# Performance work log

Measured on AMD Instinct MI355X. Metric: run time of the kernel, lower is better.

## Reference

```python
import jax, jax.numpy as jnp
import numpy as np

B, S, D, H = 2, 2048, 1024, 16
DH = D // H          # 64, even -> RoPE valid
ROPE_BASE = 10000.0
LN_EPS = 1e-5


def _rope_cache(seq_len, head_dim, dtype):
    half = head_dim // 2
    inv_freq = 1.0 / (ROPE_BASE ** (jnp.arange(half, dtype=jnp.float32) / half))
    t = jnp.arange(seq_len, dtype=jnp.float32)
    freqs = t[:, None] * inv_freq[None, :]            # [S, half]
    emb = jnp.concatenate([freqs, freqs], axis=-1)    # [S, DH]
    return jnp.cos(emb).astype(dtype)[None, None], jnp.sin(emb).astype(dtype)[None, None]


def _rotate_every_two(x):
    x_even = x[..., ::2]
    x_odd = x[..., 1::2]
    return jnp.stack([-x_odd, x_even], axis=-1).reshape(x.shape)


def setup_inputs() -> dict:
    key = jax.random.key(0)
    ks = jax.random.split(key, 4)
    w = lambda k, shape: (jax.random.normal(k, shape, jnp.float32) * 0.02)
    return {
        "x_qk": jax.random.normal(ks[0], (B, S, D), jnp.float32),
        "x_v": jax.random.normal(ks[1], (B, S, D), jnp.float32),
        "W_qk": w(ks[2], (D, 2 * D)),
        "b_qk": jnp.zeros((2 * D,), jnp.float32),
        "W_v": w(ks[3], (D, D)),
        "b_v": jnp.zeros((D,), jnp.float32),
        "ln_gamma": jnp.ones((D,), jnp.float32),
        "ln_beta": jnp.zeros((D,), jnp.float32),
    }


def reference(x_qk, x_v, W_qk, b_qk, W_v, b_v, ln_gamma, ln_beta):
    b, s, d = x_qk.shape
    # fused QK projection -> [B,S,2,H,DH]
    qk = (x_qk @ W_qk + b_qk).reshape(b, s, 2, H, DH)
    q = jnp.transpose(qk[:, :, 0], (0, 2, 1, 3))  # [B,H,S,DH]
    k = jnp.transpose(qk[:, :, 1], (0, 2, 1, 3))
    v = jnp.transpose((x_v @ W_v + b_v).reshape(b, s, H, DH), (0, 2, 1, 3))

    cos, sin = _rope_cache(s, DH, q.dtype)
    q = q * cos + _rotate_every_two(q) * sin
    k = k * cos + _rotate_every_two(k) * sin

    scale = 1.0 / jnp.sqrt(jnp.asarray(DH, q.dtype))
    scores = jnp.einsum("bhqd,bhkd->bhqk", q, k) * scale
    probs = jax.nn.softmax(scores, axis=-1)
    attn = jnp.einsum("bhqk,bhkd->bhqd", probs, v)      # [B,H,S,DH]
    attn = jnp.transpose(attn, (0, 2, 1, 3)).reshape(b, s, d)

    mu = jnp.mean(attn, axis=-1, keepdims=True)
    var = jnp.var(attn, axis=-1, keepdims=True)
    out = (attn - mu) * jax.lax.rsqrt(var + LN_EPS) * ln_gamma + ln_beta
    return out
```

## Files before the change

kernel.cpp:

```cpp
#include <hip/hip_runtime.h>
#include <hip/hip_bf16.h>

#define Bn 2
#define Sn 2048
#define Dn 1024
#define Hn 16
#define DHn 64
#define Kd 1024
#define Mn (Bn * Sn)
#define LN10K 9.210340371976184f

typedef __attribute__((ext_vector_type(8))) short bf16x8;
typedef __attribute__((ext_vector_type(4))) float f32x4;
typedef __attribute__((ext_vector_type(16))) float f32x16;

static __device__ __forceinline__ ushort f2bf(float f) {
    uint u = __float_as_uint(f);
    u += 0x7fff + ((u >> 16) & 1);
    return (ushort)(u >> 16);
}
static __device__ __forceinline__ uint cvtpk(float a, float b) {
    uint r;
    asm("v_cvt_pk_bf16_f32 %0, %1, %2" : "=v"(r) : "v"(a), "v"(b));
    return r;
}
static __device__ __forceinline__ void plswap(uint& a, uint& b) {
    asm volatile("v_permlane32_swap_b32 %0, %1" : "+v"(a), "+v"(b));
}

#define MFMA16(a, b, c) __builtin_amdgcn_mfma_f32_16x16x32_bf16((a), (b), (c), 0, 0, 0)
#define MFMA32(a, b, c) __builtin_amdgcn_mfma_f32_32x32x16_bf16((a), (b), (c), 0, 0, 0)

static __device__ __forceinline__ void gload16(const ushort* g, ushort* l) {
    __builtin_amdgcn_global_load_lds(
        (const __attribute__((address_space(1))) void*)g,
        (__attribute__((address_space(3))) void*)l, 16, 0, 0);
}

static __device__ __forceinline__ int swz(int row, int col16) {
    return row * 128 + (((col16) * 16) ^ ((row & 7) << 4));
}

__global__ __launch_bounds__(256) void rope_tab(float* __restrict__ ct,
                                                float* __restrict__ st)
{
    const int idx = blockIdx.x * 256 + threadIdx.x;
    const int s = idx >> 5, fe = idx & 31;
    const float f = expf(-LN10K * (float)fe / 32.0f);
    const float a = (float)s * f;
    ct[idx] = cosf(a);
    st[idx] = sinf(a);
}

__global__ __launch_bounds__(256) void cvt_bf16(const float* __restrict__ in,
                                                ushort* __restrict__ out)
{
    const size_t i = ((size_t)blockIdx.x * 256 + threadIdx.x) * 8;
    const float4 a = *(const float4*)(in + i);
    const float4 b = *(const float4*)(in + i + 4);
    ushort4 lo = make_ushort4(f2bf(a.x), f2bf(a.y), f2bf(a.z), f2bf(a.w));
    ushort4 hi = make_ushort4(f2bf(b.x), f2bf(b.y), f2bf(b.z), f2bf(b.w));
    *(ushort4*)(out + i) = lo;
    *(ushort4*)(out + i + 4) = hi;
}

__global__ __launch_bounds__(256) void transpose_bf16(
    const float* __restrict__ in, ushort* __restrict__ out, int R, int C)
{
    __shared__ ushort t[32][33];
    const int n0 = blockIdx.x * 32, k0 = blockIdx.y * 32;
    const int x = threadIdx.x, y = threadIdx.y;
#pragma unroll
    for (int i = 0; i < 4; ++i)
        t[y + 8 * i][x] = f2bf(in[(size_t)(k0 + y + 8 * i) * C + n0 + x]);
    __syncthreads();
#pragma unroll
    for (int i = 0; i < 4; ++i)
        out[(size_t)(n0 + y + 8 * i) * R + k0 + x] = t[x][y + 8 * i];
}

template <int MODE>
__global__ __launch_bounds__(256) void gemm_mfma(
    const ushort* __restrict__ A, const ushort* __restrict__ Bt,
    const float* __restrict__ bias, const float* __restrict__ ctab,
    const float* __restrict__ stab, ushort* __restrict__ o0,
    ushort* __restrict__ o1)
{
    __shared__ ushort Asm[128 * 64];
    __shared__ ushort Bsm[128 * 64];

    const int tid = threadIdx.x;
    const int lane = tid & 63, w = tid >> 6;
    const int g = lane >> 4, c = lane & 15;
    const int mbase = blockIdx.y * 128;
    const int nbase = blockIdx.x * 128;
    const int wm = (w >> 1) * 64, wn = (w & 1) * 64;

    f32x4 acc[4][4];
#pragma unroll
    for (int mf = 0; mf < 4; ++mf)
#pragma unroll
        for (int nf = 0; nf < 4; ++nf)
            acc[mf][nf] = (f32x4){0.f, 0.f, 0.f, 0.f};

    const int sbase = w * 64 + lane;

    for (int k0 = 0; k0 < Kd; k0 += 64) {
#pragma unroll
        for (int j = 0; j < 4; ++j) {
            const int i = j * 256 + sbase;
            const int row = i >> 3, c16 = i & 7;
            const int kc = (c16 ^ (row & 7)) * 8;
            gload16(A + (size_t)(mbase + row) * Kd + k0 + kc,
                    &Asm[(size_t)(j * 256 + w * 64) * 8]);
            gload16(Bt + (size_t)(nbase + row) * Kd + k0 + kc,
                    &Bsm[(size_t)(j * 256 + w * 64) * 8]);
        }
        __syncthreads();

#pragma unroll
        for (int ks = 0; ks < 2; ++ks) {
            bf16x8 af[4], bfr[4];
#pragma unroll
            for (int mf = 0; mf < 4; ++mf) {
                const int row = wm + mf * 16 + c;
                af[mf] = *(const bf16x8*)((const char*)Asm + swz(row, ks * 4 + g));
            }
#pragma unroll
            for (int nf = 0; nf < 4; ++nf) {
                const int row = wn + nf * 16 + c;
                bfr[nf] = *(const bf16x8*)((const char*)Bsm + swz(row, ks * 4 + g));
            }
#pragma unroll
            for (int mf = 0; mf < 4; ++mf)
#pragma unroll
                for (int nf = 0; nf < 4; ++nf)
                    acc[mf][nf] = MFMA16(af[mf], bfr[nf], acc[mf][nf]);
        }
        __syncthreads();
    }

#pragma unroll
    for (int nf = 0; nf < 4; ++nf) {
        const int col = nbase + wn + nf * 16 + c;
        const float bs = bias[col];
        if (MODE == 0) {
            const int dh = col & 63, h = (col >> 6) & 15, isK = col >> 10;
            ushort* dst = isK ? o1 : o0;
            const float sc = isK ? 1.0f : 0.18033688011112042f;
            const float* cr = ctab + (dh & 31);
            const float* sr = stab + (dh & 31);
#pragma unroll
            for (int mf = 0; mf < 4; ++mf) {
#pragma unroll
                for (int r = 0; r < 4; ++r) {
                    const int row = mbase + wm + mf * 16 + g * 4 + r;
                    const int s = row & 2047, b = row >> 11;
                    const float v = acc[mf][nf][r] + bs;
                    const float p = __shfl_xor(v, 1);
                    const float cs = cr[s * 32], sn = sr[s * 32];
                    const float ov = (c & 1) ? v * cs + p * sn
                                             : v * cs - p * sn;
                    dst[(((size_t)(b * Hn + h)) * Sn + s) * DHn + dh] =
                        f2bf(ov * sc);
                }
            }
        } else {
            const int h = col >> 6, dh = col & 63;
#pragma unroll
            for (int mf = 0; mf < 4; ++mf) {
#pragma unroll
                for (int r = 0; r < 4; ++r) {
                    const int row = mbase + wm + mf * 16 + g * 4 + r;
                    const int s = row & 2047, b = row >> 11;
                    const float v = acc[mf][nf][r] + bs;
                    o0[(((size_t)(b * Hn + h)) * DHn + dh) * Sn + s] = f2bf(v);
                }
            }
        }
    }
}

__global__ __launch_bounds__(256) void attn_mfma(
    const ushort* __restrict__ Qg, const ushort* __restrict__ Kg,
    const ushort* __restrict__ Vtg, float* __restrict__ Aw)
{
    __shared__ char Kt[3][8192];
    __shared__ char Vt[3][8192];

    const int tid = threadIdx.x;
    const int lane = tid & 63, w = tid >> 6;
    const int r31 = lane & 31, hi = lane >> 5;
    const int bh = blockIdx.y;
    const int b = bh >> 4, h = bh & 15;
    const int q0 = blockIdx.x * 128 + w * 32;

    const ushort* qp = Qg + ((size_t)bh * Sn + q0 + r31) * DHn + hi * 8;
    bf16x8 qf[4];
#pragma unroll
    for (int kt = 0; kt < 4; ++kt)
        qf[kt] = *(const bf16x8*)(qp + kt * 16);

    const short one_bf = (short)0x3F80;
    const bf16x8 ones = {one_bf, one_bf, one_bf, one_bf,
                         one_bf, one_bf, one_bf, one_bf};

    const ushort* Kb = Kg + (size_t)bh * Sn * DHn;
    const ushort* Vb = Vtg + (size_t)bh * DHn * Sn;

    auto stage = [&](int buf, int kb) {
#pragma unroll
        for (int j = 0; j < 2; ++j) {
            const int i = j * 256 + w * 64 + lane;
            const int row = i >> 3, c16 = i & 7;
            const int kc = (c16 ^ (row & 7)) * 8;
            gload16(Kb + (size_t)(kb + row) * DHn + kc,
                    (ushort*)&Kt[buf][(j * 256 + w * 64) * 16]);
            gload16(Vb + (size_t)row * Sn + kb + kc,
                    (ushort*)&Vt[buf][(j * 256 + w * 64) * 16]);
        }
    };

    stage(0, 0);
    stage(1, 64);

    f32x16 acc0, acc1, lacc;
#pragma unroll
    for (int i = 0; i < 16; ++i) { acc0[i] = 0.f; acc1[i] = 0.f; lacc[i] = 0.f; }
    float m = -1e30f;

    const int NT = Sn / 64;
    for (int t = 0; t < NT; ++t) {
        const int cur = t % 3;

        if (t < NT - 1) {
            asm volatile("s_waitcnt vmcnt(4)" ::: "memory");
        } else {
            asm volatile("s_waitcnt vmcnt(0)" ::: "memory");
        }
        __builtin_amdgcn_sched_barrier(0);
        __builtin_amdgcn_s_barrier();
        __builtin_amdgcn_sched_barrier(0);

        if (t + 2 < NT) stage((t + 2) % 3, (t + 2) * 64);
        __builtin_amdgcn_sched_barrier(0);

        f32x16 C0, C1;
#pragma unroll
        for (int i = 0; i < 16; ++i) { C0[i] = 0.f; C1[i] = 0.f; }
#pragma unroll
        for (int kt = 0; kt < 4; ++kt) {
            const bf16x8 ka = *(const bf16x8*)&Kt[cur][swz(r31, kt * 2 + hi)];
            C0 = MFMA32(ka, qf[kt], C0);
        }
#pragma unroll
        for (int kt = 0; kt < 4; ++kt) {
            const bf16x8 ka = *(const bf16x8*)&Kt[cur][swz(32 + r31, kt * 2 + hi)];
            C1 = MFMA32(ka, qf[kt], C1);
        }

        float mx[8];
#pragma unroll
        for (int i = 0; i < 8; ++i)
            mx[i] = fmaxf(fmaxf(C0[i], C0[i + 8]), fmaxf(C1[i], C1[i + 8]));
        mx[0] = fmaxf(mx[0], mx[4]); mx[1] = fmaxf(mx[1], mx[5]);
        mx[2] = fmaxf(mx[2], mx[6]); mx[3] = fmaxf(mx[3], mx[7]);
        float pmax = fmaxf(fmaxf(mx[0], mx[1]), fmaxf(mx[2], mx[3]));
        pmax = fmaxf(pmax, __shfl_xor(pmax, 32));

        if (__any(pmax > m + 11.5f)) {
            const float mn = fmaxf(m, pmax);
            const float a = exp2f(m - mn);
            m = mn;
#pragma unroll
            for (int reg = 0; reg < 16; ++reg) {
                const int qr = (reg & 3) + 8 * (reg >> 2) + 4 * hi;
                const float ar = __shfl(a, qr);
                acc0[reg] *= ar;
                acc1[reg] *= ar;
                lacc[reg] *= ar;
            }
        }

        bf16x8 paf[4];
#pragma unroll
        for (int tile = 0; tile < 2; ++tile) {
            const f32x16& C = tile ? C1 : C0;
            float e[16];
#pragma unroll
            for (int i = 0; i < 16; ++i) e[i] = exp2f(C[i] - m);
            uint p01 = cvtpk(e[0], e[1]),  p23 = cvtpk(e[2], e[3]);
            uint p45 = cvtpk(e[4], e[5]),  p67 = cvtpk(e[6], e[7]);
            uint p89 = cvtpk(e[8], e[9]),  pab = cvtpk(e[10], e[11]);
            uint pcd = cvtpk(e[12], e[13]), pef = cvtpk(e[14], e[15]);
            plswap(p01, p45); plswap(p23, p67);
            plswap(p89, pcd); plswap(pab, pef);
            uint4 f0 = {p01, p23, p45, p67};
            uint4 f1 = {p89, pab, pcd, pef};
            paf[tile * 2 + 0] = *(const bf16x8*)&f0;
            paf[tile * 2 + 1] = *(const bf16x8*)&f1;
        }

#pragma unroll
        for (int kf = 0; kf < 4; ++kf) {
            const bf16x8 v0 = *(const bf16x8*)&Vt[cur][swz(r31, kf * 2 + hi)];
            acc0 = MFMA32(paf[kf], v0, acc0);
        }
#pragma unroll
        for (int kf = 0; kf < 4; ++kf) {
            const bf16x8 v1 = *(const bf16x8*)&Vt[cur][swz(32 + r31, kf * 2 + hi)];
            acc1 = MFMA32(paf[kf], v1, acc1);
        }
#pragma unroll
        for (int kf = 0; kf < 4; ++kf)
            lacc = MFMA32(paf[kf], ones, lacc);
    }

#pragma unroll
    for (int reg = 0; reg < 16; ++reg) {
        const int qr = (reg & 3) + 8 * (reg >> 2) + 4 * hi;
        const float ir = 1.0f / lacc[reg];
        const int qs = q0 + qr;
        float* dst = &Aw[((size_t)b * Sn + qs) * Dn + h * DHn + r31];
        dst[0]  = acc0[reg] * ir;
        dst[32] = acc1[reg] * ir;
    }
}

__global__ __launch_bounds__(256) void ln_kernel(
    const float* __restrict__ Aw, const float* __restrict__ gamma,
    const float* __restrict__ beta, float* __restrict__ out)
{
    const int row = blockIdx.x;
    const int tid = threadIdx.x;
    const int d0 = tid * 4;
    const float4 x = *(const float4*)&Aw[(size_t)row * Dn + d0];
    float sum = x.x + x.y + x.z + x.w;
    float sq = x.x * x.x + x.y * x.y + x.z * x.z + x.w * x.w;
    for (int off = 32; off; off >>= 1) {
        sum += __shfl_xor(sum, off);
        sq += __shfl_xor(sq, off);
    }
    __shared__ float red[8];
    const int lane = tid & 63, wave = tid >> 6;
    if (lane == 0) { red[wave] = sum; red[wave + 4] = sq; }
    __syncthreads();
    if (tid == 0) {
        red[0] = red[0] + red[1] + red[2] + red[3];
        red[4] = red[4] + red[5] + red[6] + red[7];
    }
    __syncthreads();
    sum = red[0]; sq = red[4];
    const float mu = sum * (1.0f / Dn);
    const float var = sq * (1.0f / Dn) - mu * mu;
    const float rs = rsqrtf(var + 1e-5f);

    const float4 gv = *(const float4*)&gamma[d0];
    const float4 bv = *(const float4*)&beta[d0];
    float4 ov;
    ov.x = (x.x - mu) * rs * gv.x + bv.x;
    ov.y = (x.y - mu) * rs * gv.y + bv.y;
    ov.z = (x.z - mu) * rs * gv.z + bv.z;
    ov.w = (x.w - mu) * rs * gv.w + bv.w;
    *(float4*)&out[(size_t)row * Dn + d0] = ov;
}

extern "C" void kernel_launch(void* const* d_in, const int* in_sizes, int n_in,
                              void* d_out, int out_size, void* d_ws, size_t ws_size,
                              hipStream_t stream)
{
    const float* x_qk = (const float*)d_in[0];
    const float* x_v  = (const float*)d_in[1];
    const float* W_qk = (const float*)d_in[2];
    const float* b_qk = (const float*)d_in[3];
    const float* W_v  = (const float*)d_in[4];
    const float* b_v  = (const float*)d_in[5];
    const float* g    = (const float*)d_in[6];
    const float* be   = (const float*)d_in[7];

    char* ws = (char*)d_ws;
    ushort* Qw    = (ushort*)(ws);
    ushort* Kw    = (ushort*)(ws + (8u  << 20));
    ushort* Vtw   = (ushort*)(ws + (16u << 20));
    float*  Aw    = (float*) (ws + (24u << 20));
    ushort* xqkB  = (ushort*)(ws + (40u << 20));
    ushort* xvB   = (ushort*)(ws + (48u << 20));
    ushort* WqkT  = (ushort*)(ws + (56u << 20));
    ushort* WvT   = (ushort*)(ws + (60u << 20));
    float*  ctab  = (float*) (ws + (62u << 20));
    float*  stab  = (float*) (ws + (62u << 20) + (256u << 10));

    rope_tab<<<256, 256, 0, stream>>>(ctab, stab);
    cvt_bf16<<<2048, 256, 0, stream>>>(x_qk, xqkB);
    cvt_bf16<<<2048, 256, 0, stream>>>(x_v, xvB);
    transpose_bf16<<<dim3(64, 32), dim3(32, 8), 0, stream>>>(W_qk, WqkT, Kd, 2048);
    transpose_bf16<<<dim3(32, 32), dim3(32, 8), 0, stream>>>(W_v, WvT, Kd, 1024);

    gemm_mfma<0><<<dim3(16, 32), 256, 0, stream>>>(
        xqkB, WqkT, b_qk, ctab, stab, Qw, Kw);
    gemm_mfma<1><<<dim3(8, 32), 256, 0, stream>>>(
        xvB, WvT, b_v, ctab, stab, Vtw, nullptr);

    attn_mfma<<<dim3(16, 32), 256, 0, stream>>>(Qw, Kw, Vtw, Aw);
    ln_kernel<<<Bn * Sn, 256, 0, stream>>>(Aw, g, be, (float*)d_out);
}
```

Baseline: 170.7 us.

## Split attention KV range into two halves and merge in LayerNorm kernel

The attention kernel now processes only half of the key/value sequence per launch, and is launched twice, once per half. Each launch writes unnormalized partial outputs plus row sums and maxima, and the LayerNorm kernel combines the two halves with a log-sum-exp style rescale before normalizing. The staging buffer drops from triple to double buffering, and a minimum-occupancy launch bound is added. The two launches still run serially on one stream with the same grid size, so no extra parallelism is gained. The change also adds double partial-output traffic and combine work.

```diff
diff --git a/kernel.cpp b/kernel.cpp
--- a/kernel.cpp
+++ b/kernel.cpp
@@ -181,12 +181,13 @@
     }
 }
 
-__global__ __launch_bounds__(256) void attn_mfma(
+__global__ __launch_bounds__(256, 4) void attn_mfma(
     const ushort* __restrict__ Qg, const ushort* __restrict__ Kg,
-    const ushort* __restrict__ Vtg, float* __restrict__ Aw)
-{
-    __shared__ char Kt[3][8192];
-    __shared__ char Vt[3][8192];
+    const ushort* __restrict__ Vtg, float* __restrict__ OP,
+    float* __restrict__ Lh, float* __restrict__ Mh, int half)
+{
+    __shared__ char Kt[2][8192];
+    __shared__ char Vt[2][8192];
 
     const int tid = threadIdx.x;
     const int lane = tid & 63, w = tid >> 6;
@@ -194,6 +195,7 @@
     const int bh = blockIdx.y;
     const int b = bh >> 4, h = bh & 15;
     const int q0 = blockIdx.x * 128 + w * 32;
+    const int kvb = half * (Sn / 2);
 
     const ushort* qp = Qg + ((size_t)bh * Sn + q0 + r31) * DHn + hi * 8;
     bf16x8 qf[4];
@@ -221,28 +223,19 @@
         }
     };
 
-    stage(0, 0);
-    stage(1, 64);
+    stage(0, kvb);
 
     f32x16 acc0, acc1, lacc;
 #pragma unroll
     for (int i = 0; i < 16; ++i) { acc0[i] = 0.f; acc1[i] = 0.f; lacc[i] = 0.f; }
     float m = -1e30f;
 
-    const int NT = Sn / 64;
+    const int NT = (Sn / 2) / 64;
     for (int t = 0; t < NT; ++t) {
-        const int cur = t % 3;
-
-        if (t < NT - 1) {
-            asm volatile("s_waitcnt vmcnt(4)" ::: "memory");
-        } else {
-            asm volatile("s_waitcnt vmcnt(0)" ::: "memory");
-        }
-        __builtin_amdgcn_sched_barrier(0);
-        __builtin_amdgcn_s_barrier();
-        __builtin_amdgcn_sched_barrier(0);
-
-        if (t + 2 < NT) stage((t + 2) % 3, (t + 2) * 64);
+        const int cur = t & 1;
+
+        __syncthreads();
+        if (t + 1 < NT) stage(cur ^ 1, kvb + (t + 1) * 64);
         __builtin_amdgcn_sched_barrier(0);
 
         f32x16 C0, C1;
@@ -319,22 +312,50 @@
 #pragma unroll
     for (int reg = 0; reg < 16; ++reg) {
         const int qr = (reg & 3) + 8 * (reg >> 2) + 4 * hi;
-        const float ir = 1.0f / lacc[reg];
         const int qs = q0 + qr;
-        float* dst = &Aw[((size_t)b * Sn + qs) * Dn + h * DHn + r31];
-        dst[0]  = acc0[reg] * ir;
-        dst[32] = acc1[reg] * ir;
-    }
-}
-
-__global__ __launch_bounds__(256) void ln_kernel(
-    const float* __restrict__ Aw, const float* __restrict__ gamma,
-    const float* __restrict__ beta, float* __restrict__ out)
+        float* dst = &OP[((size_t)b * Sn + qs) * Dn + h * DHn + r31];
+        dst[0]  = acc0[reg];
+        dst[32] = acc1[reg];
+    }
+    if (r31 == 0) {
+#pragma unroll
+        for (int reg = 0; reg < 16; ++reg) {
+            const int qr = (reg & 3) + 8 * (reg >> 2) + 4 * hi;
+            Lh[(size_t)bh * Sn + q0 + qr] = lacc[reg];
+        }
+    }
+    if (hi == 0)
+        Mh[(size_t)bh * Sn + q0 + r31] = m;
+}
+
+__global__ __launch_bounds__(256) void ln_combine(
+    const float* __restrict__ OP0, const float* __restrict__ OP1,
+    const float* __restrict__ L0, const float* __restrict__ M0,
+    const float* __restrict__ L1, const float* __restrict__ M1,
+    const float* __restrict__ gamma, const float* __restrict__ beta,
+    float* __restrict__ out)
 {
     const int row = blockIdx.x;
+    const int b = row >> 11, s = row & 2047;
     const int tid = threadIdx.x;
     const int d0 = tid * 4;
-    const float4 x = *(const float4*)&Aw[(size_t)row * Dn + d0];
+    const int h = d0 >> 6;
+    const size_t idx = (size_t)(b * Hn + h) * Sn + s;
+
+    const float l0 = L0[idx], m0 = M0[idx];
+    const float l1 = L1[idx], m1 = M1[idx];
+    const float mm = fmaxf(m0, m1);
+    const float w0 = exp2f(m0 - mm), w1 = exp2f(m1 - mm);
+    const float inv = 1.0f / (l0 * w0 + l1 * w1);
+
+    const float4 o0 = *(const float4*)&OP0[(size_t)row * Dn + d0];
+    const float4 o1 = *(const float4*)&OP1[(size_t)row * Dn + d0];
+    float4 x;
+    x.x = (o0.x * w0 + o1.x * w1) * inv;
+    x.y = (o0.y * w0 + o1.y * w1) * inv;
+    x.z = (o0.z * w0 + o1.z * w1) * inv;
+    x.w = (o0.w * w0 + o1.w * w1) * inv;
+
     float sum = x.x + x.y + x.z + x.w;
     float sq = x.x * x.x + x.y * x.y + x.z * x.z + x.w * x.w;
     for (int off = 32; off; off >>= 1) {
@@ -382,11 +403,16 @@
     ushort* Qw    = (ushort*)(ws);
     ushort* Kw    = (ushort*)(ws + (8u  << 20));
     ushort* Vtw   = (ushort*)(ws + (16u << 20));
-    float*  Aw    = (float*) (ws + (24u << 20));
+    float*  OP0   = (float*) (ws + (24u << 20));
     ushort* xqkB  = (ushort*)(ws + (40u << 20));
     ushort* xvB   = (ushort*)(ws + (48u << 20));
+    float*  OP1   = (float*) (ws + (40u << 20));
     ushort* WqkT  = (ushort*)(ws + (56u << 20));
     ushort* WvT   = (ushort*)(ws + (60u << 20));
+    float*  L0    = (float*) (ws + (56u << 20));
+    float*  M0    = L0 + 65536;
+    float*  L1    = M0 + 65536;
+    float*  M1    = L1 + 65536;
     float*  ctab  = (float*) (ws + (62u << 20));
     float*  stab  = (float*) (ws + (62u << 20) + (256u << 10));
 
@@ -401,6 +427,9 @@
     gemm_mfma<1><<<dim3(8, 32), 256, 0, stream>>>(
         xvB, WvT, b_v, ctab, stab, Vtw, nullptr);
 
-    attn_mfma<<<dim3(16, 32), 256, 0, stream>>>(Qw, Kw, Vtw, Aw);
-    ln_kernel<<<Bn * Sn, 256, 0, stream>>>(Aw, g, be, (float*)d_out);
-}
+    attn_mfma<<<dim3(16, 32), 256, 0, stream>>>(Qw, Kw, Vtw, OP0, L0, M0, 0);
+    attn_mfma<<<dim3(16, 32), 256, 0, stream>>>(Qw, Kw, Vtw, OP1, L1, M1, 1);
+
+    ln_combine<<<Bn * Sn, 256, 0, stream>>>(OP0, OP1, L0, M0, L1, M1,
+                                            g, be, (float*)d_out);
+}
```

After: 206.3 us. +20.9%, slower.
